# Kernel optimization log

Hardware: AMD Instinct MI355X
Metric: run time of the kernel (lower is better)

Reference implementation:

```python
import jax, jax.numpy as jnp
import numpy as np

EMB_LEN = 1024
HEAD_SIZE = 64

def setup_inputs() -> dict:
    key = jax.random.key(0)
    k1, k2, k3, k4 = jax.random.split(key, 4)
    input_emb = jax.random.normal(k1, (8, 4096, EMB_LEN), dtype=jnp.float32)
    # nn.Linear weights are [out, in]; applied as x @ W.T
    Wq = jax.random.normal(k2, (HEAD_SIZE, EMB_LEN), dtype=jnp.float32) * (EMB_LEN ** -0.5)
    Wk = jax.random.normal(k3, (HEAD_SIZE, EMB_LEN), dtype=jnp.float32) * (EMB_LEN ** -0.5)
    Wv = jax.random.normal(k4, (HEAD_SIZE, EMB_LEN), dtype=jnp.float32) * (EMB_LEN ** -0.5)
    return {"input_emb": input_emb, "Wq": Wq, "Wk": Wk, "Wv": Wv}

def reference(input_emb, Wq, Wk, Wv):
    B, S, E = input_emb.shape
    scale = jnp.asarray(HEAD_SIZE, input_emb.dtype) ** -0.5
    q = jnp.einsum('bse,he->bsh', input_emb, Wq)  # [B,S,H]
    k = jnp.einsum('bse,he->bsh', input_emb, Wk)
    v = jnp.einsum('bse,he->bsh', input_emb, Wv)
    scores = jnp.einsum('bqh,bkh->bqk', q, k) * scale  # [B,S,S]
    causal = jnp.tril(jnp.ones((S, S), dtype=bool))
    scores = jnp.where(causal, scores, -jnp.inf)
    attn = jax.nn.softmax(scores, axis=-1)
    return jnp.einsum('bqk,bkh->bqh', attn, v)
```

## Files before the change

kernel.cpp:

```cpp
#include <hip/hip_runtime.h>
#include <hip/hip_bf16.h>

#define EMB 1024
#define HS 64
#define SEQ 4096

using bf16x8 = __attribute__((ext_vector_type(8))) __bf16;
using f32x4  = __attribute__((ext_vector_type(4))) float;
using f32x16 = __attribute__((ext_vector_type(16))) float;

__device__ __forceinline__ ushort f2b(float f) {
    unsigned x = __float_as_uint(f);
    return (ushort)((x + 0x7fffu + ((x >> 16) & 1u)) >> 16);
}

__global__ void cvt_w(const float* __restrict__ wq, const float* __restrict__ wk,
                      const float* __restrict__ wv, ushort* __restrict__ wcat) {
    int i = blockIdx.x * 256 + threadIdx.x;
    const int n = HS * EMB;
    if (i >= 3 * n) return;
    float f;
    if (i < n)          f = wq[i];
    else if (i < 2 * n) f = wk[i - n];
    else                f = wv[i - 2 * n];
    wcat[i] = f2b(f);
}

__global__ __launch_bounds__(1024) void qkv_proj(
        const float* __restrict__ x, const ushort* __restrict__ wcat,
        ushort* __restrict__ qo, ushort* __restrict__ ko, ushort* __restrict__ vo) {
    __shared__ ushort Xs[128][72];
    __shared__ ushort Ws[192][72];
    const int t = threadIdx.x;
    const int lane = t & 63, wid = t >> 6;
    const int g = lane >> 4, c = lane & 15;
    const int strip = wid >> 1, colq = wid & 1;
    const int row0 = blockIdx.x * 128;

    f32x4 acc[6];
#pragma unroll
    for (int i = 0; i < 6; ++i) acc[i] = f32x4{0.f, 0.f, 0.f, 0.f};

    for (int kc = 0; kc < EMB; kc += 64) {
        __syncthreads();
        {
            int r = t >> 3, cc = (t & 7) * 8;
            float4 v0 = *reinterpret_cast<const float4*>(&x[(size_t)(row0 + r) * EMB + kc + cc]);
            float4 v1 = *reinterpret_cast<const float4*>(&x[(size_t)(row0 + r) * EMB + kc + cc + 4]);
            ushort4 u0, u1;
            u0.x = f2b(v0.x); u0.y = f2b(v0.y); u0.z = f2b(v0.z); u0.w = f2b(v0.w);
            u1.x = f2b(v1.x); u1.y = f2b(v1.y); u1.z = f2b(v1.z); u1.w = f2b(v1.w);
            *reinterpret_cast<ushort4*>(&Xs[r][cc]) = u0;
            *reinterpret_cast<ushort4*>(&Xs[r][cc + 4]) = u1;
        }
#pragma unroll
        for (int p = 0; p < 3; ++p) {
            int wr = p * 64 + (t >> 4), wc = (t & 15) * 4;
            *reinterpret_cast<ushort4*>(&Ws[wr][wc]) =
                *reinterpret_cast<const ushort4*>(&wcat[(size_t)wr * EMB + kc + wc]);
        }
        __syncthreads();
#pragma unroll
        for (int kk = 0; kk < 2; ++kk) {
            bf16x8 a = *reinterpret_cast<const bf16x8*>(&Xs[strip * 16 + c][kk * 32 + 8 * g]);
#pragma unroll
            for (int nt = 0; nt < 6; ++nt) {
                bf16x8 b = *reinterpret_cast<const bf16x8*>(
                    &Ws[(colq * 6 + nt) * 16 + c][kk * 32 + 8 * g]);
                acc[nt] = __builtin_amdgcn_mfma_f32_16x16x32_bf16(a, b, acc[nt], 0, 0, 0);
            }
        }
    }

    const float qs = 0.125f * 1.44269504f;
#pragma unroll
    for (int nt = 0; nt < 6; ++nt) {
        int col = (colq * 6 + nt) * 16 + c;
        int rowb = row0 + strip * 16 + 4 * g;
        if (col < 64) {
#pragma unroll
            for (int r = 0; r < 4; ++r)
                qo[(rowb + r) * 64 + col] = f2b(acc[nt][r] * qs);
        } else if (col < 128) {
#pragma unroll
            for (int r = 0; r < 4; ++r)
                ko[(rowb + r) * 64 + (col - 64)] = f2b(acc[nt][r]);
        } else {
            int b = rowb >> 12, s0 = rowb & 4095;
            ushort4 pv;
            pv.x = f2b(acc[nt][0]); pv.y = f2b(acc[nt][1]);
            pv.z = f2b(acc[nt][2]); pv.w = f2b(acc[nt][3]);
            *reinterpret_cast<ushort4*>(&vo[(b * 64 + (col - 128)) * SEQ + s0]) = pv;
        }
    }
}

__global__ __launch_bounds__(256) void attn(
        const ushort* __restrict__ q, const ushort* __restrict__ k,
        const ushort* __restrict__ vt, float* __restrict__ out, float* __restrict__ L) {
    __shared__ __align__(16) char smem[32768];

    const int t = threadIdx.x;
    const int lane = t & 63, w = t >> 6;
    const int ql = lane & 31, h = lane >> 5;

    const int batch = blockIdx.x & 7;
    const int x = 143 - (int)(blockIdx.x >> 3);
    int gi = 0;
#pragma unroll
    for (int g2 = 1; g2 <= 7; ++g2) if (x >= 2 * g2 * (g2 + 1)) gi = g2;
    const int off = x - 2 * gi * (gi + 1);
    const int ns = gi + 1;
    const int j = off / ns;
    const int seg = off - j * ns;
    const int qt = 4 * gi + j;
    const int T = 2 * (qt + 1);
    const int Td = T / ns, Tr = T % ns;
    const int t0 = seg * Td + (seg < Tr ? seg : Tr);
    const int tcnt = Td + (seg < Tr ? 1 : 0);

    const int q0w = qt * 128 + w * 32;

    const ushort* qb = q + (size_t)batch * SEQ * 64;
    const ushort* kb = k + (size_t)batch * SEQ * 64;
    const ushort* vb = vt + (size_t)batch * 64 * SEQ;

    bf16x8 qa[4];
#pragma unroll
    for (int ks = 0; ks < 4; ++ks)
        qa[ks] = *reinterpret_cast<const bf16x8*>(&qb[(q0w + ql) * 64 + ks * 16 + 8 * h]);

    f32x16 accO0, accO1;
#pragma unroll
    for (int r = 0; r < 16; ++r) { accO0[r] = 0.f; accO1[r] = 0.f; }
    float lsum = 0.f;

    auto stage = [&](int tile, int buf) {
        const int kv0 = tile * 64;
#pragma unroll
        for (int n = 0; n < 4; ++n) {
            const int fid = w * 4 + n;
            const ushort* src;
            if (fid < 8)
                src = &kb[(size_t)(kv0 + (fid >> 2) * 32 + ql) * 64 + (fid & 3) * 16 + 8 * h];
            else
                src = &vb[(size_t)(((fid - 8) >> 2) * 32 + ql) * SEQ + kv0 + ((fid - 8) & 3) * 16 + 8 * h];
            char* dst = smem + buf * 16384 + fid * 1024 + lane * 16;
            __builtin_amdgcn_global_load_lds(
                (const __attribute__((address_space(1))) void*)src,
                (__attribute__((address_space(3))) void*)dst, 16, 0, 0);
        }
    };

    stage(t0, 0);

    for (int ti = 0; ti < tcnt; ++ti) {
        asm volatile("s_waitcnt vmcnt(0)" ::: "memory");
        __builtin_amdgcn_s_barrier();
        __builtin_amdgcn_sched_barrier(0);
        if (ti + 1 < tcnt) stage(t0 + ti + 1, (ti + 1) & 1);

        const char* kbase = smem + (ti & 1) * 16384;
        const char* vbase = kbase + 8192;
        const int kv0 = (t0 + ti) * 64;
        const bool cross = (kv0 + 64 > q0w);

#pragma unroll
        for (int kt2 = 0; kt2 < 2; ++kt2) {
            f32x16 S;
#pragma unroll
            for (int r = 0; r < 16; ++r) S[r] = 0.f;
#pragma unroll
            for (int ks = 0; ks < 4; ++ks) {
                bf16x8 kf = *reinterpret_cast<const bf16x8*>(kbase + (kt2 * 4 + ks) * 1024 + lane * 16);
                S = __builtin_amdgcn_mfma_f32_32x32x16_bf16(kf, qa[ks], S, 0, 0, 0);
            }
            if (cross) {
#pragma unroll
                for (int r = 0; r < 16; ++r) {
                    int kv = kv0 + kt2 * 32 + (r & 3) + 8 * (r >> 2) + 4 * h;
                    if (kv > q0w + ql) S[r] = -INFINITY;
                }
            }
            uint d0, d1, d2, d3, d4, d5, d6, d7;
            {
                float p[16];
#pragma unroll
                for (int r = 0; r < 16; ++r) {
                    p[r] = __builtin_amdgcn_exp2f(S[r]);
                    lsum += p[r];
                }
                asm("v_cvt_pk_bf16_f32 %0, %1, %2" : "=v"(d0) : "v"(p[0]),  "v"(p[1]));
                asm("v_cvt_pk_bf16_f32 %0, %1, %2" : "=v"(d1) : "v"(p[2]),  "v"(p[3]));
                asm("v_cvt_pk_bf16_f32 %0, %1, %2" : "=v"(d2) : "v"(p[4]),  "v"(p[5]));
                asm("v_cvt_pk_bf16_f32 %0, %1, %2" : "=v"(d3) : "v"(p[6]),  "v"(p[7]));
                asm("v_cvt_pk_bf16_f32 %0, %1, %2" : "=v"(d4) : "v"(p[8]),  "v"(p[9]));
                asm("v_cvt_pk_bf16_f32 %0, %1, %2" : "=v"(d5) : "v"(p[10]), "v"(p[11]));
                asm("v_cvt_pk_bf16_f32 %0, %1, %2" : "=v"(d6) : "v"(p[12]), "v"(p[13]));
                asm("v_cvt_pk_bf16_f32 %0, %1, %2" : "=v"(d7) : "v"(p[14]), "v"(p[15]));
            }
#pragma unroll
            for (int kk = 0; kk < 2; ++kk) {
                uint a0 = kk ? d4 : d0, a1 = kk ? d5 : d1;
                uint b0 = kk ? d6 : d2, b1 = kk ? d7 : d3;
                asm("v_permlane32_swap_b32 %0, %1" : "+v"(a0), "+v"(b0));
                asm("v_permlane32_swap_b32 %0, %1" : "+v"(a1), "+v"(b1));
                uint pw[4] = {a0, a1, b0, b1};
                bf16x8 pa = *reinterpret_cast<bf16x8*>(pw);
                const int kk2 = kt2 * 2 + kk;
                bf16x8 vf0 = *reinterpret_cast<const bf16x8*>(vbase + (0 * 4 + kk2) * 1024 + lane * 16);
                bf16x8 vf1 = *reinterpret_cast<const bf16x8*>(vbase + (1 * 4 + kk2) * 1024 + lane * 16);
                accO0 = __builtin_amdgcn_mfma_f32_32x32x16_bf16(pa, vf0, accO0, 0, 0, 0);
                accO1 = __builtin_amdgcn_mfma_f32_32x32x16_bf16(pa, vf1, accO1, 0, 0, 0);
            }
        }
    }

    lsum += __shfl_xor(lsum, 32, 64);
    float* ob = out + (size_t)batch * SEQ * 64;
#pragma unroll
    for (int r = 0; r < 16; ++r) {
        int qrow = q0w + (r & 3) + 8 * (r >> 2) + 4 * h;
        atomicAdd(&ob[(size_t)qrow * 64 + ql], accO0[r]);
        atomicAdd(&ob[(size_t)qrow * 64 + 32 + ql], accO1[r]);
    }
    if (h == 0) atomicAdd(&L[batch * SEQ + q0w + ql], lsum);
}

__global__ __launch_bounds__(256) void norm_out(float* __restrict__ out,
                                                const float* __restrict__ L) {
    int i = blockIdx.x * 256 + threadIdx.x;
    float4 v = reinterpret_cast<float4*>(out)[i];
    float li = L[i >> 4];
    float inv = (li > 0.f) ? 1.0f / li : 0.f;
    v.x *= inv; v.y *= inv; v.z *= inv; v.w *= inv;
    reinterpret_cast<float4*>(out)[i] = v;
}

extern "C" void kernel_launch(void* const* d_in, const int* in_sizes, int n_in,
                              void* d_out, int out_size, void* d_ws, size_t ws_size,
                              hipStream_t stream) {
    const float* x  = (const float*)d_in[0];
    const float* wq = (const float*)d_in[1];
    const float* wk = (const float*)d_in[2];
    const float* wv = (const float*)d_in[3];
    float* out = (float*)d_out;

    char* ws = (char*)d_ws;
    ushort* wcat = (ushort*)ws;
    ushort* qo   = (ushort*)(ws + 393216);
    ushort* ko   = (ushort*)(ws + 393216 + 4194304);
    ushort* vo   = (ushort*)(ws + 393216 + 2 * 4194304);
    float*  Lb   = (float*)(ws + 393216 + 3 * 4194304);

    hipMemsetAsync(out, 0, (size_t)8 * SEQ * 64 * 4, stream);
    hipMemsetAsync(Lb, 0, (size_t)8 * SEQ * 4, stream);
    hipLaunchKernelGGL(cvt_w, dim3(768), dim3(256), 0, stream, wq, wk, wv, wcat);
    hipLaunchKernelGGL(qkv_proj, dim3(256), dim3(1024), 0, stream, x, wcat, qo, ko, vo);
    hipLaunchKernelGGL(attn, dim3(1152), dim3(256), 0, stream, qo, ko, vo, out, Lb);
    hipLaunchKernelGGL(norm_out, dim3(2048), dim3(256), 0, stream, out, Lb);
}
```

Baseline: 103.3 us.

## Drop LDS staging in QKV projection; waves load X and W directly

Rewrites the QKV projection so each wave independently computes a 16-row by 96-column tile, loading fp32 X rows and bf16 weights straight from global memory into MFMA operands. It removes shared-memory staging and per-chunk block barriers, and uses packed bf16 conversion instructions. It launches more, smaller blocks with an occupancy hint. The cost is losing LDS reuse: X is fetched by two waves and W by every wave, so it leans on caches, and the global access pattern is less coalesced.

```diff
diff --git a/kernel.cpp b/kernel.cpp
--- a/kernel.cpp
+++ b/kernel.cpp
@@ -26,57 +26,47 @@
     wcat[i] = f2b(f);
 }
 
-__global__ __launch_bounds__(1024) void qkv_proj(
+__global__ __launch_bounds__(256, 4) void qkv_proj(
         const float* __restrict__ x, const ushort* __restrict__ wcat,
         ushort* __restrict__ qo, ushort* __restrict__ ko, ushort* __restrict__ vo) {
-    __shared__ ushort Xs[128][72];
-    __shared__ ushort Ws[192][72];
     const int t = threadIdx.x;
-    const int lane = t & 63, wid = t >> 6;
+    const int lane = t & 63, w = t >> 6;
     const int g = lane >> 4, c = lane & 15;
-    const int strip = wid >> 1, colq = wid & 1;
-    const int row0 = blockIdx.x * 128;
+    const int wid = blockIdx.x * 4 + w;
+    const int row0 = (wid >> 1) * 16;
+    const int nh = wid & 1;
 
     f32x4 acc[6];
 #pragma unroll
     for (int i = 0; i < 6; ++i) acc[i] = f32x4{0.f, 0.f, 0.f, 0.f};
 
-    for (int kc = 0; kc < EMB; kc += 64) {
-        __syncthreads();
-        {
-            int r = t >> 3, cc = (t & 7) * 8;
-            float4 v0 = *reinterpret_cast<const float4*>(&x[(size_t)(row0 + r) * EMB + kc + cc]);
-            float4 v1 = *reinterpret_cast<const float4*>(&x[(size_t)(row0 + r) * EMB + kc + cc + 4]);
-            ushort4 u0, u1;
-            u0.x = f2b(v0.x); u0.y = f2b(v0.y); u0.z = f2b(v0.z); u0.w = f2b(v0.w);
-            u1.x = f2b(v1.x); u1.y = f2b(v1.y); u1.z = f2b(v1.z); u1.w = f2b(v1.w);
-            *reinterpret_cast<ushort4*>(&Xs[r][cc]) = u0;
-            *reinterpret_cast<ushort4*>(&Xs[r][cc + 4]) = u1;
-        }
-#pragma unroll
-        for (int p = 0; p < 3; ++p) {
-            int wr = p * 64 + (t >> 4), wc = (t & 15) * 4;
-            *reinterpret_cast<ushort4*>(&Ws[wr][wc]) =
-                *reinterpret_cast<const ushort4*>(&wcat[(size_t)wr * EMB + kc + wc]);
-        }
-        __syncthreads();
-#pragma unroll
-        for (int kk = 0; kk < 2; ++kk) {
-            bf16x8 a = *reinterpret_cast<const bf16x8*>(&Xs[strip * 16 + c][kk * 32 + 8 * g]);
-#pragma unroll
-            for (int nt = 0; nt < 6; ++nt) {
-                bf16x8 b = *reinterpret_cast<const bf16x8*>(
-                    &Ws[(colq * 6 + nt) * 16 + c][kk * 32 + 8 * g]);
-                acc[nt] = __builtin_amdgcn_mfma_f32_16x16x32_bf16(a, b, acc[nt], 0, 0, 0);
-            }
+    const float* xr = x + (size_t)(row0 + c) * EMB;
+    const size_t wrow0 = (size_t)(nh * 96 + c) * EMB;
+
+#pragma unroll 2
+    for (int kk = 0; kk < 32; ++kk) {
+        const int k0 = kk * 32 + 8 * g;
+        float4 xa = *reinterpret_cast<const float4*>(&xr[k0]);
+        float4 xb = *reinterpret_cast<const float4*>(&xr[k0 + 4]);
+        uint pw[4];
+        asm("v_cvt_pk_bf16_f32 %0, %1, %2" : "=v"(pw[0]) : "v"(xa.x), "v"(xa.y));
+        asm("v_cvt_pk_bf16_f32 %0, %1, %2" : "=v"(pw[1]) : "v"(xa.z), "v"(xa.w));
+        asm("v_cvt_pk_bf16_f32 %0, %1, %2" : "=v"(pw[2]) : "v"(xb.x), "v"(xb.y));
+        asm("v_cvt_pk_bf16_f32 %0, %1, %2" : "=v"(pw[3]) : "v"(xb.z), "v"(xb.w));
+        bf16x8 a = *reinterpret_cast<bf16x8*>(pw);
+
+#pragma unroll
+        for (int nt = 0; nt < 6; ++nt) {
+            bf16x8 b = *reinterpret_cast<const bf16x8*>(&wcat[wrow0 + (size_t)nt * 16 * EMB + k0]);
+            acc[nt] = __builtin_amdgcn_mfma_f32_16x16x32_bf16(a, b, acc[nt], 0, 0, 0);
         }
     }
 
     const float qs = 0.125f * 1.44269504f;
 #pragma unroll
     for (int nt = 0; nt < 6; ++nt) {
-        int col = (colq * 6 + nt) * 16 + c;
-        int rowb = row0 + strip * 16 + 4 * g;
+        int col = (nh * 6 + nt) * 16 + c;
+        int rowb = row0 + 4 * g;
         if (col < 64) {
 #pragma unroll
             for (int r = 0; r < 4; ++r)
@@ -256,7 +246,7 @@
     hipMemsetAsync(out, 0, (size_t)8 * SEQ * 64 * 4, stream);
     hipMemsetAsync(Lb, 0, (size_t)8 * SEQ * 4, stream);
     hipLaunchKernelGGL(cvt_w, dim3(768), dim3(256), 0, stream, wq, wk, wv, wcat);
-    hipLaunchKernelGGL(qkv_proj, dim3(256), dim3(1024), 0, stream, x, wcat, qo, ko, vo);
+    hipLaunchKernelGGL(qkv_proj, dim3(1024), dim3(256), 0, stream, x, wcat, qo, ko, vo);
     hipLaunchKernelGGL(attn, dim3(1152), dim3(256), 0, stream, qo, ko, vo, out, Lb);
     hipLaunchKernelGGL(norm_out, dim3(2048), dim3(256), 0, stream, out, Lb);
 }
```

Result: slower. 178.3 us (+72.6%).
